# Performance work log

Hardware: AMD Instinct MI355X
Metric: run time of the kernel (lower is better)

The kernel has to match this reference:

```python
import jax, jax.numpy as jnp
import numpy as np

N_STATE = 64
N_OBS = 32
N_IN = 16
T = 1024
DT = 0.01

# Dopri5 Butcher tableau (same as diffrax.Dopri5)
_A_TAB = [
    [],
    [1/5],
    [3/40, 9/40],
    [44/45, -56/15, 32/9],
    [19372/6561, -25360/2187, 64448/6561, -212/729],
    [9017/3168, -355/33, 46732/5247, 49/176, -5103/18656],
    [35/384, 0.0, 500/1113, 125/192, -2187/6784, 11/84],
]
_C_TAB = [0.0, 1/5, 3/10, 4/5, 8/9, 1.0, 1.0]
_B_TAB = [35/384, 0.0, 500/1113, 125/192, -2187/6784, 11/84, 0.0]


def setup_inputs() -> dict:
    key = jax.random.key(0)
    ks = jax.random.split(key, 6)
    ts = jnp.arange(T, dtype=jnp.float32) * DT
    ys = jax.random.normal(ks[0], (T, N_OBS), jnp.float32)
    us = jax.random.normal(ks[1], (T, N_IN), jnp.float32)
    # stable system matrix so the Riccati ODE stays bounded
    A = 0.1 * jax.random.normal(ks[2], (N_STATE, N_STATE), jnp.float32) - jnp.eye(N_STATE, dtype=jnp.float32)
    B = 0.1 * jax.random.normal(ks[3], (N_STATE, N_IN), jnp.float32)
    C = 0.1 * jax.random.normal(ks[4], (N_OBS, N_STATE), jnp.float32)
    x0 = jax.random.normal(ks[5], (N_STATE,), jnp.float32)
    P0 = jnp.eye(N_STATE, dtype=jnp.float32)
    Q = 0.01 * jnp.eye(N_STATE, dtype=jnp.float32)
    R = 0.1 * jnp.eye(N_OBS, dtype=jnp.float32)
    return {"ts": ts, "ys": ys, "us": us, "A": A, "B": B, "C": C,
            "x0": x0, "P0": P0, "Q": Q, "R": R}


def reference(ts, ys, us, A, B, C, x0, P0, Q, R):
    h = ts[1] - ts[0]  # constant step == save spacing (dt0)
    nT = ys.shape[0]
    Rinv = jnp.linalg.inv(R)  # R is constant; original inverts it each rhs eval
    Ct = C.T

    def interp(arr, t):
        # linear interpolation on the uniform grid ts
        s = (t - ts[0]) / h
        i0 = jnp.clip(jnp.floor(s).astype(jnp.int32), 0, nT - 2)
        w = s - i0.astype(s.dtype)
        return arr[i0] * (1.0 - w) + arr[i0 + 1] * w

    def rhs(t, x, P):
        PCtRi = P @ Ct @ Rinv                      # Kalman gain K, [n,p]
        dP = A @ P + P @ A.T + Q - PCtRi @ (C @ P)  # Riccati ODE
        dx = A @ x + B @ interp(us, t) + PCtRi @ (interp(ys, t) - C @ x)
        return dx, dP

    def step(carry, t):
        x, P = carry
        kx, kP = [], []
        for i in range(7):  # fixed 7-stage RK, unrolled
            xi, Pi = x, P
            for j, aij in enumerate(_A_TAB[i]):
                if aij != 0.0:
                    xi = xi + (h * aij) * kx[j]
                    Pi = Pi + (h * aij) * kP[j]
            dx, dP = rhs(t + _C_TAB[i] * h, xi, Pi)
            kx.append(dx)
            kP.append(dP)
        xn, Pn = x, P
        for i, bi in enumerate(_B_TAB):
            if bi != 0.0:
                xn = xn + (h * bi) * kx[i]
                Pn = Pn + (h * bi) * kP[i]
        return (xn, Pn), xn

    (_, _), xs = jax.lax.scan(step, (x0, P0), ts[:-1])
    return jnp.concatenate([x0[None], xs], axis=0)  # [T, n] filtered states
```

## Files before the change

kernel.cpp:

```cpp
#include <hip/hip_runtime.h>

typedef float f32x4 __attribute__((ext_vector_type(4)));
typedef short s16x8 __attribute__((ext_vector_type(8)));
typedef short s16x4 __attribute__((ext_vector_type(4)));

namespace kf {
constexpr int TN = 1024, NS = 64, NO = 32, NI = 16;
constexpr int PP = 72;
constexpr int PK = 40;
constexpr int PKP = 68;

constexpr float ATAB[6][5] = {
  {0.f,0.f,0.f,0.f,0.f},
  {(float)(1.0/5.0),0.f,0.f,0.f,0.f},
  {(float)(3.0/40.0),(float)(9.0/40.0),0.f,0.f,0.f},
  {(float)(44.0/45.0),(float)(-56.0/15.0),(float)(32.0/9.0),0.f,0.f},
  {(float)(19372.0/6561.0),(float)(-25360.0/2187.0),(float)(64448.0/6561.0),(float)(-212.0/729.0),0.f},
  {(float)(9017.0/3168.0),(float)(-355.0/33.0),(float)(46732.0/5247.0),(float)(49.0/176.0),(float)(-5103.0/18656.0)},
};
constexpr float CTAB[6] = {0.f,(float)(1.0/5.0),(float)(3.0/10.0),(float)(4.0/5.0),(float)(8.0/9.0),1.f};
constexpr float BW0=(float)(35.0/384.0), BW2=(float)(500.0/1113.0), BW3=(float)(125.0/192.0),
                BW4=(float)(-2187.0/6784.0), BW5=(float)(11.0/84.0);

struct ShB {
  unsigned short Pib[80*PP];
  unsigned short Ab [64*PP];
  unsigned short Cb [32*PP];
  unsigned short RCb[32*PP];
  unsigned short KKb[64*PK];
  unsigned short GTb[80*PK];
  float Bf[64*16];
  float BUB[2][64];
  float KXL[5][64];
  float FAC[32];
  int HYP;
};
constexpr size_t SH_BASE  = (sizeof(ShB) + 255) & ~size_t(255);
constexpr size_t SH_TOTAL = SH_BASE + size_t(5*64*PKP)*4;
}
using namespace kf;

__device__ inline float bf2f(unsigned short u){
  unsigned int x = ((unsigned int)u) << 16; return __builtin_bit_cast(float, x);
}
__device__ inline unsigned short f2bf(float f){
  unsigned int x = __builtin_bit_cast(unsigned int, f);
  return (unsigned short)((x + 0x7fffu + ((x >> 16) & 1u)) >> 16);
}
__device__ __forceinline__ unsigned int pack2bf(float a, float b){
  return (unsigned int)f2bf(a) | ((unsigned int)f2bf(b) << 16);
}
__device__ inline s16x8 load_frag(const unsigned short* arr, int pitch, int row0, int k0, int hyp){
  const int l = (int)(threadIdx.x & 63), lc = l & 15, lg = l >> 4;
  const unsigned short* p = arr + (row0 + lc) * pitch + k0;
  if ((hyp & 1) == 0) {
    return *(const s16x8*)(p + lg * 8);
  } else {
    s16x4 a = *(const s16x4*)(p + lg * 4);
    s16x4 b = *(const s16x4*)(p + 16 + lg * 4);
    s16x8 r; r[0]=a[0]; r[1]=a[1]; r[2]=a[2]; r[3]=a[3]; r[4]=b[0]; r[5]=b[1]; r[6]=b[2]; r[7]=b[3];
    return r;
  }
}
__device__ inline f32x4 MF(s16x8 a, s16x8 b, f32x4 c, int hyp){
  if (hyp & 2) return __builtin_amdgcn_mfma_f32_16x16x32_bf16(b, a, c, 0, 0, 0);
  return __builtin_amdgcn_mfma_f32_16x16x32_bf16(a, b, c, 0, 0, 0);
}
template<int HYP>
__device__ __forceinline__ s16x8 load_fragT(const unsigned short* arr, int pitch, int row0, int k0){
  const int l = (int)(threadIdx.x & 63), lc = l & 15, lg = l >> 4;
  const unsigned short* p = arr + (row0 + lc) * pitch + k0;
  if constexpr ((HYP & 1) == 0) {
    return *(const s16x8*)(p + lg * 8);
  } else {
    s16x4 a = *(const s16x4*)(p + lg * 4);
    s16x4 b = *(const s16x4*)(p + 16 + lg * 4);
    s16x8 r; r[0]=a[0]; r[1]=a[1]; r[2]=a[2]; r[3]=a[3]; r[4]=b[0]; r[5]=b[1]; r[6]=b[2]; r[7]=b[3];
    return r;
  }
}
template<int HYP>
__device__ __forceinline__ f32x4 MFT(s16x8 a, s16x8 b, f32x4 c){
  if constexpr ((HYP & 2) != 0) return __builtin_amdgcn_mfma_f32_16x16x32_bf16(b, a, c, 0, 0, 0);
  else                          return __builtin_amdgcn_mfma_f32_16x16x32_bf16(a, b, c, 0, 0, 0);
}

template<int HYP>
__device__ __forceinline__ void scan_body(ShB& sh, float* __restrict__ KPL,
    const float* __restrict__ ts, const float* __restrict__ ys, const float* __restrict__ us,
    const float* __restrict__ x0g, const float* __restrict__ P0g, const float* __restrict__ Qg,
    float* __restrict__ out)
{
  const int tid = (int)threadIdx.x;
  const int w = tid >> 6, l = tid & 63;
  const int lc = l & 15, lg = l >> 4;
  const int sr = w & 3, ch = w >> 2;
  const int rowbase = 16*sr + 4*lg;
  const bool isx = (ch == 0);
  const bool isg = (sr == 3);

  const float h = ts[1] - ts[0];
  f32x4 z4 = {0.f,0.f,0.f,0.f};
  f32x4 Pfr[2], Qfr[2], AP[2], APdX, XRv;
  s16x8 aA[2], aRC[2], aC[2], bA[2][2];
  f32x4 y1v = z4, y2v = z4;
  #pragma unroll
  for (int c2 = 0; c2 < 2; ++c2) { Pfr[c2]=z4; Qfr[c2]=z4; AP[c2]=z4; }
  APdX = z4;

  #pragma unroll
  for (int c2 = 0; c2 < 2; ++c2)
    #pragma unroll
    for (int r = 0; r < 4; ++r) {
      int row = 16*sr + 4*lg + r, col = 16*(2*ch + c2) + lc;
      Pfr[c2][r] = P0g[row*64 + col];
      Qfr[c2][r] = Qg [row*64 + col];
    }
  #pragma unroll
  for (int kb = 0; kb < 2; ++kb) {
    aA [kb] = load_fragT<HYP>(sh.Ab,  PP, 16*sr, 32*kb);
    aRC[kb] = load_fragT<HYP>(sh.RCb, PP, 16*ch, 32*kb);
    aC [kb] = load_fragT<HYP>(sh.Cb,  PP, 16*ch, 32*kb);
    #pragma unroll
    for (int c2 = 0; c2 < 2; ++c2)
      bA[c2][kb] = load_fragT<HYP>(sh.Ab, PP, 16*(2*ch + c2), 32*kb);
  }
  XRv = *(const f32x4*)&x0g[rowbase];
  if (isg) {
    y1v = *(const f32x4*)&ys[16*ch + 4*lg];
    y2v = *(const f32x4*)&ys[NO + 16*ch + 4*lg];
  }
  if (tid < 64) {
    out[tid] = x0g[tid];
    sh.Pib[64*PP + tid] = f2bf(x0g[tid]);
    const f32x4* bf4 = (const f32x4*)&sh.Bf[tid*16];
    const f32x4* up4 = (const f32x4*)us;
    float bu = 0.f;
    #pragma unroll
    for (int m4 = 0; m4 < 4; ++m4) {
      f32x4 b = bf4[m4], u = up4[m4];
      bu += b.x*u.x + b.y*u.y + b.z*u.z + b.w*u.w;
    }
    sh.BUB[0][tid] = bu;
  }
  for (int idx = tid; idx < 15*PP; idx += 512) sh.Pib[65*PP + idx] = 0;
  if (tid < PP - 64) sh.Pib[64*PP + 64 + tid] = 0;
  for (int idx = tid; idx < 16*PK; idx += 512) sh.GTb[64*PK + idx] = 0;
  __syncthreads();

  for (int t = 0; t < TN - 1; ++t) {
    #pragma unroll
    for (int st = 0; st < 6; ++st) {
      if (t > 0 || st > 0) {
        s16x8 am = load_fragT<HYP>(sh.KKb, PK, 16*sr, 0);
        #pragma unroll
        for (int c2 = 0; c2 < 2; ++c2) {
          const int ct = 2*ch + c2;
          s16x8 bg = load_fragT<HYP>(sh.GTb, PK, 16*ct, 0);
          f32x4 kPv = MFT<HYP>(am, bg, AP[c2]);
          float* kbase = &KPL[(size_t)(16*ct + lc) * PKP + 16*sr + 4*lg];
          f32x4 x;
          if (st == 0) {
            f32x4 k0v = *(const f32x4*)(kbase + 0*64*PKP);
            f32x4 k2v = *(const f32x4*)(kbase + 2*64*PKP);
            f32x4 k3v = *(const f32x4*)(kbase + 3*64*PKP);
            f32x4 k4v = *(const f32x4*)(kbase + 4*64*PKP);
            #pragma unroll
            for (int r = 0; r < 4; ++r)
              Pfr[c2][r] += h * (BW0*k0v[r] + BW2*k2v[r] + BW3*k3v[r]
                               + BW4*k4v[r] + BW5*kPv[r] + Qfr[c2][r]);
            x = Pfr[c2];
          } else {
            *(f32x4*)(kbase + (size_t)(st-1)*64*PKP) = kPv;
            #pragma unroll
            for (int r = 0; r < 4; ++r)
              x[r] = Pfr[c2][r] + (h * CTAB[st]) * Qfr[c2][r] + (h * ATAB[st][st-1]) * kPv[r];
            if (st >= 2) { f32x4 kv = *(const f32x4*)(kbase + 0*64*PKP);
              #pragma unroll
              for (int r = 0; r < 4; ++r) x[r] += (h * ATAB[st][0]) * kv[r]; }
            if (st >= 3) { f32x4 kv = *(const f32x4*)(kbase + 1*64*PKP);
              #pragma unroll
              for (int r = 0; r < 4; ++r) x[r] += (h * ATAB[st][1]) * kv[r]; }
            if (st >= 4) { f32x4 kv = *(const f32x4*)(kbase + 2*64*PKP);
              #pragma unroll
              for (int r = 0; r < 4; ++r) x[r] += (h * ATAB[st][2]) * kv[r]; }
            if (st >= 5) { f32x4 kv = *(const f32x4*)(kbase + 3*64*PKP);
              #pragma unroll
              for (int r = 0; r < 4; ++r) x[r] += (h * ATAB[st][3]) * kv[r]; }
          }
          uint2 pk; pk.x = pack2bf(x[0], x[1]); pk.y = pack2bf(x[2], x[3]);
          *(uint2*)&sh.Pib[(16*ct + lc)*PP + 16*sr + 4*lg] = pk;
        }
        if (isx) {
          s16x8 bgX = load_fragT<HYP>(sh.GTb, PK, 64, 0);
          f32x4 kx = MFT<HYP>(am, bgX, APdX);
          {
            f32x4 bu1 = *(const f32x4*)&sh.BUB[t & 1][rowbase];
            if (st == 0) {
              kx += bu1;
            } else {
              const float cp = CTAB[st-1];
              if (cp != 0.f) {
                f32x4 bu2 = *(const f32x4*)&sh.BUB[(t + 1) & 1][rowbase];
                kx += (1.f - cp) * bu1 + cp * bu2;
              } else {
                kx += bu1;
              }
            }
          }
          f32x4 xiv;
          if (st == 0) {
            f32x4 k0 = *(const f32x4*)&sh.KXL[0][rowbase];
            f32x4 k2 = *(const f32x4*)&sh.KXL[2][rowbase];
            f32x4 k3 = *(const f32x4*)&sh.KXL[3][rowbase];
            f32x4 k4 = *(const f32x4*)&sh.KXL[4][rowbase];
            XRv += h * (BW0*k0 + BW2*k2 + BW3*k3 + BW4*k4 + BW5*kx);
            if (lc == 0) *(f32x4*)&out[(size_t)t*64 + rowbase] = XRv;
            xiv = XRv;
          } else {
            if (lc == 0) *(f32x4*)&sh.KXL[st-1][rowbase] = kx;
            xiv = XRv + (h * ATAB[st][st-1]) * kx;
            if (st >= 2 && ATAB[st][0] != 0.f) xiv += (h * ATAB[st][0]) * (*(const f32x4*)&sh.KXL[0][rowbase]);
            if (st >= 3 && ATAB[st][1] != 0.f) xiv += (h * ATAB[st][1]) * (*(const f32x4*)&sh.KXL[1][rowbase]);
            if (st >= 4 && ATAB[st][2] != 0.f) xiv += (h * ATAB[st][2]) * (*(const f32x4*)&sh.KXL[2][rowbase]);
            if (st >= 5 && ATAB[st][3] != 0.f) xiv += (h * ATAB[st][3]) * (*(const f32x4*)&sh.KXL[3][rowbase]);
          }
          if (lc == 0) {
            uint2 pk; pk.x = pack2bf(xiv[0], xiv[1]); pk.y = pack2bf(xiv[2], xiv[3]);
            *(uint2*)&sh.Pib[64*PP + rowbase] = pk;
          }
        }
      } else {
        #pragma unroll
        for (int c2 = 0; c2 < 2; ++c2) {
          const int ct = 2*ch + c2;
          uint2 pk; pk.x = pack2bf(Pfr[c2][0], Pfr[c2][1]); pk.y = pack2bf(Pfr[c2][2], Pfr[c2][3]);
          *(uint2*)&sh.Pib[(16*ct + lc)*PP + 16*sr + 4*lg] = pk;
        }
      }
      __syncthreads();
      {
        s16x8 aPi0 = load_fragT<HYP>(sh.Pib, PP, 16*sr, 0);
        s16x8 aPi1 = load_fragT<HYP>(sh.Pib, PP, 16*sr, 32);
        #pragma unroll
        for (int c2 = 0; c2 < 2; ++c2) {
          const int ct = 2*ch + c2;
          s16x8 bP0 = load_fragT<HYP>(sh.Pib, PP, 16*ct, 0);
          s16x8 bP1 = load_fragT<HYP>(sh.Pib, PP, 16*ct, 32);
          f32x4 acc = MFT<HYP>(aA[0], bP0, z4);
          acc = MFT<HYP>(aA[1], bP1, acc);
          acc = MFT<HYP>(aPi0, bA[c2][0], acc);
          AP[c2] = MFT<HYP>(aPi1, bA[c2][1], acc);
        }
        f32x4 aK = MFT<HYP>(aRC[1], aPi1, MFT<HYP>(aRC[0], aPi0, z4));
        uint2 pkk; pkk.x = pack2bf(aK[0], aK[1]); pkk.y = pack2bf(aK[2], aK[3]);
        *(uint2*)&sh.KKb[(16*sr + lc)*PK + 16*ch + 4*lg] = pkk;
        f32x4 aG = MFT<HYP>(aC[1], aPi1, MFT<HYP>(aC[0], aPi0, z4));
        uint2 pkg; pkg.x = pack2bf(aG[0], aG[1]); pkg.y = pack2bf(aG[2], aG[3]);
        *(uint2*)&sh.GTb[(16*sr + lc)*PK + 16*ch + 4*lg] = pkg;
      }
      if (isx || isg) {
        s16x8 px0 = load_fragT<HYP>(sh.Pib, PP, 64, 0);
        s16x8 px1 = load_fragT<HYP>(sh.Pib, PP, 64, 32);
        if (isx) {
          APdX = MFT<HYP>(aA[1], px1, MFT<HYP>(aA[0], px0, z4));
        }
        if (isg) {
          f32x4 gx = MFT<HYP>(aC[1], px1, MFT<HYP>(aC[0], px0, z4));
          const float c = CTAB[st];
          f32x4 v;
          #pragma unroll
          for (int r = 0; r < 4; ++r) {
            float yc = (1.f - c) * y1v[r] + c * y2v[r];
            v[r] = gx[r] - yc;
          }
          uint2 pk;
          if (lc == 0) { pk.x = pack2bf(v[0], v[1]); pk.y = pack2bf(v[2], v[3]); }
          else         { pk.x = 0u; pk.y = 0u; }
          *(uint2*)&sh.GTb[(64 + lc)*PK + 16*ch + 4*lg] = pk;
        }
      }
      if (st == 0 && tid < 64) {
        const f32x4* bf4 = (const f32x4*)&sh.Bf[tid*16];
        const f32x4* up4 = (const f32x4*)(us + (size_t)(t + 1)*NI);
        float bu = 0.f;
        #pragma unroll
        for (int m4 = 0; m4 < 4; ++m4) {
          f32x4 b = bf4[m4], u = up4[m4];
          bu += b.x*u.x + b.y*u.y + b.z*u.z + b.w*u.w;
        }
        sh.BUB[(t + 1) & 1][tid] = bu;
      }
      __syncthreads();
    }
    if (isg) {
      y1v = y2v;
      if (t + 2 < TN) y2v = *(const f32x4*)&ys[(size_t)(t + 2)*NO + 16*ch + 4*lg];
    }
  }

  if (isx) {
    s16x8 am  = load_fragT<HYP>(sh.KKb, PK, 16*sr, 0);
    s16x8 bgX = load_fragT<HYP>(sh.GTb, PK, 64, 0);
    f32x4 kx = MFT<HYP>(am, bgX, APdX);
    kx += *(const f32x4*)&sh.BUB[(TN - 1) & 1][rowbase];
    f32x4 k0 = *(const f32x4*)&sh.KXL[0][rowbase];
    f32x4 k2 = *(const f32x4*)&sh.KXL[2][rowbase];
    f32x4 k3 = *(const f32x4*)&sh.KXL[3][rowbase];
    f32x4 k4 = *(const f32x4*)&sh.KXL[4][rowbase];
    XRv += h * (BW0*k0 + BW2*k2 + BW3*k3 + BW4*k4 + BW5*kx);
    if (lc == 0) *(f32x4*)&out[(size_t)(TN - 1)*64 + rowbase] = XRv;
  }
}

__global__ __launch_bounds__(512, 1)
void kf_mfma12(const float* __restrict__ ts, const float* __restrict__ ys,
               const float* __restrict__ us, const float* __restrict__ Ag,
               const float* __restrict__ Bg, const float* __restrict__ Cg,
               const float* __restrict__ x0g, const float* __restrict__ P0g,
               const float* __restrict__ Qg, const float* __restrict__ Rg,
               float* __restrict__ out)
{
  extern __shared__ char dsm[];
  ShB& sh = *(ShB*)dsm;
  float* KPL = (float*)(dsm + SH_BASE);
  float* GJ  = KPL;
  const int tid = (int)threadIdx.x;
  const int wv = tid >> 6;
  const int lc = tid & 15, lg = (tid & 63) >> 4;

  for (int idx = tid; idx < 64*64; idx += 512) sh.Ab[(idx>>6)*PP + (idx&63)] = f2bf(Ag[idx]);
  for (int idx = tid; idx < 32*64; idx += 512) sh.Cb[(idx>>6)*PP + (idx&63)] = f2bf(Cg[idx]);
  for (int idx = tid; idx < 64*16; idx += 512) sh.Bf[idx] = Bg[idx];
  for (int idx = tid; idx < 32*64; idx += 512) {
    int r = idx >> 6, c = idx & 63;
    GJ[idx] = (c < 32) ? Rg[r*32 + c] : ((c - 32) == r ? 1.f : 0.f);
  }
  __syncthreads();
  for (int k2 = 0; k2 < 32; ++k2) {
    if (tid < 32) sh.FAC[tid] = GJ[tid*64 + k2];
    __syncthreads();
    const float pinv = 1.f / sh.FAC[k2];
    float oldv[4], vk[4];
    #pragma unroll
    for (int s = 0; s < 4; ++s) {
      int idx = tid + s*512;
      oldv[s] = GJ[idx];
      vk[s]   = GJ[k2*64 + (idx & 63)];
    }
    __syncthreads();
    #pragma unroll
    for (int s = 0; s < 4; ++s) {
      int idx = tid + s*512, i = idx >> 6;
      GJ[idx] = (i == k2) ? (oldv[s] * pinv) : (oldv[s] - sh.FAC[i] * (vk[s] * pinv));
    }
    __syncthreads();
  }
  for (int idx = tid; idx < 32*64; idx += 512) {
    int q = idx >> 6, k = idx & 63;
    float a = 0.f;
    for (int p = 0; p < 32; ++p) a += GJ[q*64 + 32 + p] * Cg[p*64 + k];
    sh.RCb[q*PP + k] = f2bf(-a);
  }
  __syncthreads();
  __shared__ float Xref[256];
  if (tid < 256) {
    int r = tid >> 4, c = tid & 15;
    float a = 0.f;
    for (int k = 0; k < 32; ++k) a += bf2f(sh.Ab[r*PP + k]) * bf2f(sh.Ab[(16 + c)*PP + k]);
    Xref[tid] = a;
  }
  if (tid == 0) sh.HYP = -1;
  __syncthreads();
  for (int hh = 0; hh < 4; ++hh) {
    if (wv == 0) {
      s16x8 af = load_frag(sh.Ab, PP, 0, 0, hh);
      s16x8 bf = load_frag(sh.Ab, PP, 16, 0, hh);
      f32x4 z = {0.f,0.f,0.f,0.f};
      f32x4 d = MF(af, bf, z, hh);
      int ok = 1;
      #pragma unroll
      for (int r = 0; r < 4; ++r) {
        float rf = Xref[(lg*4 + r)*16 + lc];
        ok &= (fabsf(d[r] - rf) <= 1e-3f + 1e-2f * fabsf(rf)) ? 1 : 0;
      }
      if (__all(ok) && tid == 0) { if (sh.HYP < 0) sh.HYP = hh; }
    }
    __syncthreads();
  }
  const int sHyp = (sh.HYP < 0) ? 0 : sh.HYP;

  switch (sHyp) {
    case 0: scan_body<0>(sh, KPL, ts, ys, us, x0g, P0g, Qg, out); break;
    case 1: scan_body<1>(sh, KPL, ts, ys, us, x0g, P0g, Qg, out); break;
    case 2: scan_body<2>(sh, KPL, ts, ys, us, x0g, P0g, Qg, out); break;
    default: scan_body<3>(sh, KPL, ts, ys, us, x0g, P0g, Qg, out); break;
  }
}

extern "C" void kernel_launch(void* const* d_in, const int* in_sizes, int n_in,
                              void* d_out, int out_size, void* d_ws, size_t ws_size,
                              hipStream_t stream) {
  (void)in_sizes; (void)n_in; (void)out_size; (void)d_ws; (void)ws_size;
  const float* ts  = (const float*)d_in[0];
  const float* ys  = (const float*)d_in[1];
  const float* us  = (const float*)d_in[2];
  const float* A   = (const float*)d_in[3];
  const float* B   = (const float*)d_in[4];
  const float* C   = (const float*)d_in[5];
  const float* x0  = (const float*)d_in[6];
  const float* P0  = (const float*)d_in[7];
  const float* Q   = (const float*)d_in[8];
  const float* R   = (const float*)d_in[9];
  (void)hipFuncSetAttribute(reinterpret_cast<const void*>(kf_mfma12),
                            hipFuncAttributeMaxDynamicSharedMemorySize, (int)SH_TOTAL);
  hipLaunchKernelGGL(kf_mfma12, dim3(1), dim3(512), SH_TOTAL, stream,
                     ts, ys, us, A, B, C, x0, P0, Q, R, (float*)d_out);
}
```

Baseline: 7.169 ms.

## Split Riccati scan over 16 waves and keep RK stage slopes in registers

```diff
diff --git a/kernel.cpp b/kernel.cpp
--- a/kernel.cpp
+++ b/kernel.cpp
@@ -8,7 +8,6 @@
 constexpr int TN = 1024, NS = 64, NO = 32, NI = 16;
 constexpr int PP = 72;
 constexpr int PK = 40;
-constexpr int PKP = 68;
 
 constexpr float ATAB[6][5] = {
   {0.f,0.f,0.f,0.f,0.f},
@@ -31,12 +30,9 @@
   unsigned short GTb[80*PK];
   float Bf[64*16];
   float BUB[2][64];
-  float KXL[5][64];
   float FAC[32];
   int HYP;
 };
-constexpr size_t SH_BASE  = (sizeof(ShB) + 255) & ~size_t(255);
-constexpr size_t SH_TOTAL = SH_BASE + size_t(5*64*PKP)*4;
 }
 using namespace kf;
 
@@ -86,44 +82,40 @@
 }
 
 template<int HYP>
-__device__ __forceinline__ void scan_body(ShB& sh, float* __restrict__ KPL,
+__device__ __forceinline__ void scan_body(ShB& sh,
     const float* __restrict__ ts, const float* __restrict__ ys, const float* __restrict__ us,
     const float* __restrict__ x0g, const float* __restrict__ P0g, const float* __restrict__ Qg,
     float* __restrict__ out)
 {
   const int tid = (int)threadIdx.x;
-  const int w = tid >> 6, l = tid & 63;
+  const int wid = tid >> 6, l = tid & 63;
   const int lc = l & 15, lg = l >> 4;
-  const int sr = w & 3, ch = w >> 2;
+  const int sr = wid >> 2, cq = wid & 3;
+  const int ch = (cq < 2) ? cq : (cq - 2);
   const int rowbase = 16*sr + 4*lg;
-  const bool isx = (ch == 0);
-  const bool isg = (sr == 3);
+  const bool isx = (cq == 0);
+  const bool isg = (sr == 3) && (cq >= 2);
 
   const float h = ts[1] - ts[0];
   f32x4 z4 = {0.f,0.f,0.f,0.f};
-  f32x4 Pfr[2], Qfr[2], AP[2], APdX, XRv;
-  s16x8 aA[2], aRC[2], aC[2], bA[2][2];
+  f32x4 Pfr, Qfr, AP = z4, APdX = z4, XRv;
+  f32x4 kP0=z4,kP1=z4,kP2=z4,kP3=z4,kP4=z4;
+  f32x4 kx0=z4,kx1=z4,kx2=z4,kx3=z4,kx4=z4;
+  s16x8 aA[2], bA[2], aW[2];
   f32x4 y1v = z4, y2v = z4;
+
   #pragma unroll
-  for (int c2 = 0; c2 < 2; ++c2) { Pfr[c2]=z4; Qfr[c2]=z4; AP[c2]=z4; }
-  APdX = z4;
-
-  #pragma unroll
-  for (int c2 = 0; c2 < 2; ++c2)
-    #pragma unroll
-    for (int r = 0; r < 4; ++r) {
-      int row = 16*sr + 4*lg + r, col = 16*(2*ch + c2) + lc;
-      Pfr[c2][r] = P0g[row*64 + col];
-      Qfr[c2][r] = Qg [row*64 + col];
-    }
+  for (int r = 0; r < 4; ++r) {
+    int row = rowbase + r, col = 16*cq + lc;
+    Pfr[r] = P0g[row*64 + col];
+    Qfr[r] = Qg [row*64 + col];
+  }
   #pragma unroll
   for (int kb = 0; kb < 2; ++kb) {
-    aA [kb] = load_fragT<HYP>(sh.Ab,  PP, 16*sr, 32*kb);
-    aRC[kb] = load_fragT<HYP>(sh.RCb, PP, 16*ch, 32*kb);
-    aC [kb] = load_fragT<HYP>(sh.Cb,  PP, 16*ch, 32*kb);
-    #pragma unroll
-    for (int c2 = 0; c2 < 2; ++c2)
-      bA[c2][kb] = load_fragT<HYP>(sh.Ab, PP, 16*(2*ch + c2), 32*kb);
+    aA[kb] = load_fragT<HYP>(sh.Ab, PP, 16*sr, 32*kb);
+    bA[kb] = load_fragT<HYP>(sh.Ab, PP, 16*cq, 32*kb);
+    if (cq < 2) aW[kb] = load_fragT<HYP>(sh.RCb, PP, 16*ch, 32*kb);
+    else        aW[kb] = load_fragT<HYP>(sh.Cb,  PP, 16*ch, 32*kb);
   }
   XRv = *(const f32x4*)&x0g[rowbase];
   if (isg) {
@@ -143,9 +135,9 @@
     }
     sh.BUB[0][tid] = bu;
   }
-  for (int idx = tid; idx < 15*PP; idx += 512) sh.Pib[65*PP + idx] = 0;
+  for (int idx = tid; idx < 15*PP; idx += 1024) sh.Pib[65*PP + idx] = 0;
   if (tid < PP - 64) sh.Pib[64*PP + 64 + tid] = 0;
-  for (int idx = tid; idx < 16*PK; idx += 512) sh.GTb[64*PK + idx] = 0;
+  for (int idx = tid; idx < 16*PK; idx += 1024) sh.GTb[64*PK + idx] = 0;
   __syncthreads();
 
   for (int t = 0; t < TN - 1; ++t) {
@@ -153,44 +145,23 @@
     for (int st = 0; st < 6; ++st) {
       if (t > 0 || st > 0) {
         s16x8 am = load_fragT<HYP>(sh.KKb, PK, 16*sr, 0);
-        #pragma unroll
-        for (int c2 = 0; c2 < 2; ++c2) {
-          const int ct = 2*ch + c2;
-          s16x8 bg = load_fragT<HYP>(sh.GTb, PK, 16*ct, 0);
-          f32x4 kPv = MFT<HYP>(am, bg, AP[c2]);
-          float* kbase = &KPL[(size_t)(16*ct + lc) * PKP + 16*sr + 4*lg];
-          f32x4 x;
-          if (st == 0) {
-            f32x4 k0v = *(const f32x4*)(kbase + 0*64*PKP);
-            f32x4 k2v = *(const f32x4*)(kbase + 2*64*PKP);
-            f32x4 k3v = *(const f32x4*)(kbase + 3*64*PKP);
-            f32x4 k4v = *(const f32x4*)(kbase + 4*64*PKP);
-            #pragma unroll
-            for (int r = 0; r < 4; ++r)
-              Pfr[c2][r] += h * (BW0*k0v[r] + BW2*k2v[r] + BW3*k3v[r]
-                               + BW4*k4v[r] + BW5*kPv[r] + Qfr[c2][r]);
-            x = Pfr[c2];
-          } else {
-            *(f32x4*)(kbase + (size_t)(st-1)*64*PKP) = kPv;
-            #pragma unroll
-            for (int r = 0; r < 4; ++r)
-              x[r] = Pfr[c2][r] + (h * CTAB[st]) * Qfr[c2][r] + (h * ATAB[st][st-1]) * kPv[r];
-            if (st >= 2) { f32x4 kv = *(const f32x4*)(kbase + 0*64*PKP);
-              #pragma unroll
-              for (int r = 0; r < 4; ++r) x[r] += (h * ATAB[st][0]) * kv[r]; }
-            if (st >= 3) { f32x4 kv = *(const f32x4*)(kbase + 1*64*PKP);
-              #pragma unroll
-              for (int r = 0; r < 4; ++r) x[r] += (h * ATAB[st][1]) * kv[r]; }
-            if (st >= 4) { f32x4 kv = *(const f32x4*)(kbase + 2*64*PKP);
-              #pragma unroll
-              for (int r = 0; r < 4; ++r) x[r] += (h * ATAB[st][2]) * kv[r]; }
-            if (st >= 5) { f32x4 kv = *(const f32x4*)(kbase + 3*64*PKP);
-              #pragma unroll
-              for (int r = 0; r < 4; ++r) x[r] += (h * ATAB[st][3]) * kv[r]; }
-          }
-          uint2 pk; pk.x = pack2bf(x[0], x[1]); pk.y = pack2bf(x[2], x[3]);
-          *(uint2*)&sh.Pib[(16*ct + lc)*PP + 16*sr + 4*lg] = pk;
+        s16x8 bg = load_fragT<HYP>(sh.GTb, PK, 16*cq, 0);
+        f32x4 kPv = MFT<HYP>(am, bg, AP);
+        f32x4 x;
+        if (st == 0) {
+          Pfr += h * (BW0*kP0 + BW2*kP2 + BW3*kP3 + BW4*kP4 + BW5*kPv + Qfr);
+          x = Pfr;
+        } else {
+          x = Pfr + (h * CTAB[st]) * Qfr + (h * ATAB[st][st-1]) * kPv;
+          if (st >= 2) x += (h * ATAB[st][0]) * kP0;
+          if (st >= 3) x += (h * ATAB[st][1]) * kP1;
+          if (st >= 4) x += (h * ATAB[st][2]) * kP2;
+          if (st >= 5) x += (h * ATAB[st][3]) * kP3;
+          if (st == 1) kP0 = kPv; else if (st == 2) kP1 = kPv;
+          else if (st == 3) kP2 = kPv; else if (st == 4) kP3 = kPv; else kP4 = kPv;
         }
+        uint2 pk; pk.x = pack2bf(x[0], x[1]); pk.y = pack2bf(x[2], x[3]);
+        *(uint2*)&sh.Pib[(16*cq + lc)*PP + rowbase] = pk;
         if (isx) {
           s16x8 bgX = load_fragT<HYP>(sh.GTb, PK, 64, 0);
           f32x4 kx = MFT<HYP>(am, bgX, APdX);
@@ -210,63 +181,49 @@
           }
           f32x4 xiv;
           if (st == 0) {
-            f32x4 k0 = *(const f32x4*)&sh.KXL[0][rowbase];
-            f32x4 k2 = *(const f32x4*)&sh.KXL[2][rowbase];
-            f32x4 k3 = *(const f32x4*)&sh.KXL[3][rowbase];
-            f32x4 k4 = *(const f32x4*)&sh.KXL[4][rowbase];
-            XRv += h * (BW0*k0 + BW2*k2 + BW3*k3 + BW4*k4 + BW5*kx);
+            XRv += h * (BW0*kx0 + BW2*kx2 + BW3*kx3 + BW4*kx4 + BW5*kx);
             if (lc == 0) *(f32x4*)&out[(size_t)t*64 + rowbase] = XRv;
             xiv = XRv;
           } else {
-            if (lc == 0) *(f32x4*)&sh.KXL[st-1][rowbase] = kx;
             xiv = XRv + (h * ATAB[st][st-1]) * kx;
-            if (st >= 2 && ATAB[st][0] != 0.f) xiv += (h * ATAB[st][0]) * (*(const f32x4*)&sh.KXL[0][rowbase]);
-            if (st >= 3 && ATAB[st][1] != 0.f) xiv += (h * ATAB[st][1]) * (*(const f32x4*)&sh.KXL[1][rowbase]);
-            if (st >= 4 && ATAB[st][2] != 0.f) xiv += (h * ATAB[st][2]) * (*(const f32x4*)&sh.KXL[2][rowbase]);
-            if (st >= 5 && ATAB[st][3] != 0.f) xiv += (h * ATAB[st][3]) * (*(const f32x4*)&sh.KXL[3][rowbase]);
+            if (st >= 2 && ATAB[st][0] != 0.f) xiv += (h * ATAB[st][0]) * kx0;
+            if (st >= 3 && ATAB[st][1] != 0.f) xiv += (h * ATAB[st][1]) * kx1;
+            if (st >= 4 && ATAB[st][2] != 0.f) xiv += (h * ATAB[st][2]) * kx2;
+            if (st >= 5 && ATAB[st][3] != 0.f) xiv += (h * ATAB[st][3]) * kx3;
+            if (st == 1) kx0 = kx; else if (st == 2) kx1 = kx;
+            else if (st == 3) kx2 = kx; else if (st == 4) kx3 = kx; else kx4 = kx;
           }
           if (lc == 0) {
-            uint2 pk; pk.x = pack2bf(xiv[0], xiv[1]); pk.y = pack2bf(xiv[2], xiv[3]);
-            *(uint2*)&sh.Pib[64*PP + rowbase] = pk;
+            uint2 pk2; pk2.x = pack2bf(xiv[0], xiv[1]); pk2.y = pack2bf(xiv[2], xiv[3]);
+            *(uint2*)&sh.Pib[64*PP + rowbase] = pk2;
           }
         }
       } else {
-        #pragma unroll
-        for (int c2 = 0; c2 < 2; ++c2) {
-          const int ct = 2*ch + c2;
-          uint2 pk; pk.x = pack2bf(Pfr[c2][0], Pfr[c2][1]); pk.y = pack2bf(Pfr[c2][2], Pfr[c2][3]);
-          *(uint2*)&sh.Pib[(16*ct + lc)*PP + 16*sr + 4*lg] = pk;
-        }
+        uint2 pk; pk.x = pack2bf(Pfr[0], Pfr[1]); pk.y = pack2bf(Pfr[2], Pfr[3]);
+        *(uint2*)&sh.Pib[(16*cq + lc)*PP + rowbase] = pk;
       }
       __syncthreads();
       {
         s16x8 aPi0 = load_fragT<HYP>(sh.Pib, PP, 16*sr, 0);
         s16x8 aPi1 = load_fragT<HYP>(sh.Pib, PP, 16*sr, 32);
-        #pragma unroll
-        for (int c2 = 0; c2 < 2; ++c2) {
-          const int ct = 2*ch + c2;
-          s16x8 bP0 = load_fragT<HYP>(sh.Pib, PP, 16*ct, 0);
-          s16x8 bP1 = load_fragT<HYP>(sh.Pib, PP, 16*ct, 32);
-          f32x4 acc = MFT<HYP>(aA[0], bP0, z4);
-          acc = MFT<HYP>(aA[1], bP1, acc);
-          acc = MFT<HYP>(aPi0, bA[c2][0], acc);
-          AP[c2] = MFT<HYP>(aPi1, bA[c2][1], acc);
-        }
-        f32x4 aK = MFT<HYP>(aRC[1], aPi1, MFT<HYP>(aRC[0], aPi0, z4));
-        uint2 pkk; pkk.x = pack2bf(aK[0], aK[1]); pkk.y = pack2bf(aK[2], aK[3]);
-        *(uint2*)&sh.KKb[(16*sr + lc)*PK + 16*ch + 4*lg] = pkk;
-        f32x4 aG = MFT<HYP>(aC[1], aPi1, MFT<HYP>(aC[0], aPi0, z4));
-        uint2 pkg; pkg.x = pack2bf(aG[0], aG[1]); pkg.y = pack2bf(aG[2], aG[3]);
-        *(uint2*)&sh.GTb[(16*sr + lc)*PK + 16*ch + 4*lg] = pkg;
+        s16x8 bP0  = load_fragT<HYP>(sh.Pib, PP, 16*cq, 0);
+        s16x8 bP1  = load_fragT<HYP>(sh.Pib, PP, 16*cq, 32);
+        f32x4 acc = MFT<HYP>(aA[0], bP0, z4);
+        acc = MFT<HYP>(aA[1], bP1, acc);
+        acc = MFT<HYP>(aPi0, bA[0], acc);
+        AP  = MFT<HYP>(aPi1, bA[1], acc);
+        f32x4 aKG = MFT<HYP>(aW[1], aPi1, MFT<HYP>(aW[0], aPi0, z4));
+        uint2 pkk; pkk.x = pack2bf(aKG[0], aKG[1]); pkk.y = pack2bf(aKG[2], aKG[3]);
+        if (cq < 2) *(uint2*)&sh.KKb[(16*sr + lc)*PK + 16*ch + 4*lg] = pkk;
+        else        *(uint2*)&sh.GTb[(16*sr + lc)*PK + 16*ch + 4*lg] = pkk;
       }
       if (isx || isg) {
         s16x8 px0 = load_fragT<HYP>(sh.Pib, PP, 64, 0);
         s16x8 px1 = load_fragT<HYP>(sh.Pib, PP, 64, 32);
         if (isx) {
           APdX = MFT<HYP>(aA[1], px1, MFT<HYP>(aA[0], px0, z4));
-        }
-        if (isg) {
-          f32x4 gx = MFT<HYP>(aC[1], px1, MFT<HYP>(aC[0], px0, z4));
+        } else {
+          f32x4 gx = MFT<HYP>(aW[1], px1, MFT<HYP>(aW[0], px0, z4));
           const float c = CTAB[st];
           f32x4 v;
           #pragma unroll
@@ -280,8 +237,8 @@
           *(uint2*)&sh.GTb[(64 + lc)*PK + 16*ch + 4*lg] = pk;
         }
       }
-      if (st == 0 && tid < 64) {
-        const f32x4* bf4 = (const f32x4*)&sh.Bf[tid*16];
+      if (st == 0 && wid == 1) {
+        const f32x4* bf4 = (const f32x4*)&sh.Bf[l*16];
         const f32x4* up4 = (const f32x4*)(us + (size_t)(t + 1)*NI);
         float bu = 0.f;
         #pragma unroll
@@ -289,7 +246,7 @@
           f32x4 b = bf4[m4], u = up4[m4];
           bu += b.x*u.x + b.y*u.y + b.z*u.z + b.w*u.w;
         }
-        sh.BUB[(t + 1) & 1][tid] = bu;
+        sh.BUB[(t + 1) & 1][l] = bu;
       }
       __syncthreads();
     }
@@ -304,35 +261,30 @@
     s16x8 bgX = load_fragT<HYP>(sh.GTb, PK, 64, 0);
     f32x4 kx = MFT<HYP>(am, bgX, APdX);
     kx += *(const f32x4*)&sh.BUB[(TN - 1) & 1][rowbase];
-    f32x4 k0 = *(const f32x4*)&sh.KXL[0][rowbase];
-    f32x4 k2 = *(const f32x4*)&sh.KXL[2][rowbase];
-    f32x4 k3 = *(const f32x4*)&sh.KXL[3][rowbase];
-    f32x4 k4 = *(const f32x4*)&sh.KXL[4][rowbase];
-    XRv += h * (BW0*k0 + BW2*k2 + BW3*k3 + BW4*k4 + BW5*kx);
+    XRv += h * (BW0*kx0 + BW2*kx2 + BW3*kx3 + BW4*kx4 + BW5*kx);
     if (lc == 0) *(f32x4*)&out[(size_t)(TN - 1)*64 + rowbase] = XRv;
   }
 }
 
-__global__ __launch_bounds__(512, 1)
-void kf_mfma12(const float* __restrict__ ts, const float* __restrict__ ys,
+__global__ __launch_bounds__(1024, 1)
+void kf_mfma13(const float* __restrict__ ts, const float* __restrict__ ys,
                const float* __restrict__ us, const float* __restrict__ Ag,
                const float* __restrict__ Bg, const float* __restrict__ Cg,
                const float* __restrict__ x0g, const float* __restrict__ P0g,
                const float* __restrict__ Qg, const float* __restrict__ Rg,
                float* __restrict__ out)
 {
-  extern __shared__ char dsm[];
-  ShB& sh = *(ShB*)dsm;
-  float* KPL = (float*)(dsm + SH_BASE);
-  float* GJ  = KPL;
+  __shared__ ShB sh;
+  __shared__ float Xref[256];
+  float* GJ = (float*)sh.KKb;
   const int tid = (int)threadIdx.x;
   const int wv = tid >> 6;
   const int lc = tid & 15, lg = (tid & 63) >> 4;
 
-  for (int idx = tid; idx < 64*64; idx += 512) sh.Ab[(idx>>6)*PP + (idx&63)] = f2bf(Ag[idx]);
-  for (int idx = tid; idx < 32*64; idx += 512) sh.Cb[(idx>>6)*PP + (idx&63)] = f2bf(Cg[idx]);
-  for (int idx = tid; idx < 64*16; idx += 512) sh.Bf[idx] = Bg[idx];
-  for (int idx = tid; idx < 32*64; idx += 512) {
+  for (int idx = tid; idx < 64*64; idx += 1024) sh.Ab[(idx>>6)*PP + (idx&63)] = f2bf(Ag[idx]);
+  for (int idx = tid; idx < 32*64; idx += 1024) sh.Cb[(idx>>6)*PP + (idx&63)] = f2bf(Cg[idx]);
+  for (int idx = tid; idx < 64*16; idx += 1024) sh.Bf[idx] = Bg[idx];
+  for (int idx = tid; idx < 32*64; idx += 1024) {
     int r = idx >> 6, c = idx & 63;
     GJ[idx] = (c < 32) ? Rg[r*32 + c] : ((c - 32) == r ? 1.f : 0.f);
   }
@@ -341,29 +293,28 @@
     if (tid < 32) sh.FAC[tid] = GJ[tid*64 + k2];
     __syncthreads();
     const float pinv = 1.f / sh.FAC[k2];
-    float oldv[4], vk[4];
+    float oldv[2], vk[2];
     #pragma unroll
-    for (int s = 0; s < 4; ++s) {
-      int idx = tid + s*512;
+    for (int s = 0; s < 2; ++s) {
+      int idx = tid + s*1024;
       oldv[s] = GJ[idx];
       vk[s]   = GJ[k2*64 + (idx & 63)];
     }
     __syncthreads();
     #pragma unroll
-    for (int s = 0; s < 4; ++s) {
-      int idx = tid + s*512, i = idx >> 6;
+    for (int s = 0; s < 2; ++s) {
+      int idx = tid + s*1024, i = idx >> 6;
       GJ[idx] = (i == k2) ? (oldv[s] * pinv) : (oldv[s] - sh.FAC[i] * (vk[s] * pinv));
     }
     __syncthreads();
   }
-  for (int idx = tid; idx < 32*64; idx += 512) {
+  for (int idx = tid; idx < 32*64; idx += 1024) {
     int q = idx >> 6, k = idx & 63;
     float a = 0.f;
     for (int p = 0; p < 32; ++p) a += GJ[q*64 + 32 + p] * Cg[p*64 + k];
     sh.RCb[q*PP + k] = f2bf(-a);
   }
   __syncthreads();
-  __shared__ float Xref[256];
   if (tid < 256) {
     int r = tid >> 4, c = tid & 15;
     float a = 0.f;
@@ -391,10 +342,10 @@
   const int sHyp = (sh.HYP < 0) ? 0 : sh.HYP;
 
   switch (sHyp) {
-    case 0: scan_body<0>(sh, KPL, ts, ys, us, x0g, P0g, Qg, out); break;
-    case 1: scan_body<1>(sh, KPL, ts, ys, us, x0g, P0g, Qg, out); break;
-    case 2: scan_body<2>(sh, KPL, ts, ys, us, x0g, P0g, Qg, out); break;
-    default: scan_body<3>(sh, KPL, ts, ys, us, x0g, P0g, Qg, out); break;
+    case 0: scan_body<0>(sh, ts, ys, us, x0g, P0g, Qg, out); break;
+    case 1: scan_body<1>(sh, ts, ys, us, x0g, P0g, Qg, out); break;
+    case 2: scan_body<2>(sh, ts, ys, us, x0g, P0g, Qg, out); break;
+    default: scan_body<3>(sh, ts, ys, us, x0g, P0g, Qg, out); break;
   }
 }
 
@@ -412,8 +363,6 @@
   const float* P0  = (const float*)d_in[7];
   const float* Q   = (const float*)d_in[8];
   const float* R   = (const float*)d_in[9];
-  (void)hipFuncSetAttribute(reinterpret_cast<const void*>(kf_mfma12),
-                            hipFuncAttributeMaxDynamicSharedMemorySize, (int)SH_TOTAL);
-  hipLaunchKernelGGL(kf_mfma12, dim3(1), dim3(512), SH_TOTAL, stream,
+  hipLaunchKernelGGL(kf_mfma13, dim3(1), dim3(1024), 0, stream,
                      ts, ys, us, A, B, C, x0, P0, Q, R, (float*)d_out);
 }
```

After: 15.59 ms. 2.17x slower.
